# Optimization experiments

Measured on AMD Instinct MI355X. Metric: run time of the kernel, lower is better.

## Reference

```python
import jax, jax.numpy as jnp
import numpy as np

TAU = 0.07
EPS = 1e-10


def setup_inputs() -> dict:
    key = jax.random.key(0)
    k1, k2 = jax.random.split(key)
    N, D = 8192, 128
    features = jax.random.normal(k1, (N, D), dtype=jnp.float32)
    alpha = jnp.float32(0.5)  # cosine-similarity threshold in (-1, 1)
    return {"features": features, "alpha": alpha}


def reference(features, alpha):
    # L2-normalize rows (torch F.normalize uses eps=1e-12 clamp on the norm)
    norm = jnp.maximum(jnp.linalg.norm(features, axis=1, keepdims=True), 1e-12)
    f = features / norm
    sim = f @ f.T  # [N, N]

    n = f.shape[0]
    not_eye = ~jnp.eye(n, dtype=bool)
    pos_mask = (sim >= alpha) & not_eye
    neg_mask = (sim < alpha) & not_eye

    e = jnp.exp(sim / TAU)  # [N, N], computed once and reused for both masks
    numerator = jnp.sum(jnp.where(pos_mask, e, 0.0), axis=1) + EPS
    denominator = numerator + jnp.sum(jnp.where(neg_mask, e, 0.0), axis=1) + EPS
    loss = -jnp.log(numerator / denominator)
    return loss.mean()
```

## Files before the change

### kernel.cpp

```cpp
#include <hip/hip_runtime.h>

#define N_ROWS 8192
#define DIM 128
#define BM 128
#define CHUNK 1024
#define BN 64
#define NITER (CHUNK/BN)
#define NCHUNK (N_ROWS/CHUNK)

typedef __attribute__((ext_vector_type(8))) short short8;
typedef __attribute__((ext_vector_type(4))) float f32x4;

__device__ __forceinline__ void gload_lds16(const void* g, void* l) {
  __builtin_amdgcn_global_load_lds(
      (const __attribute__((address_space(1))) void*)g,
      (__attribute__((address_space(3))) void*)l, 16, 0, 0);
}

__device__ __forceinline__ unsigned short f2bf(float x) {
  unsigned int u = __float_as_uint(x);
  unsigned int r = (u + 0x7fffu + ((u >> 16) & 1u)) >> 16;
  return (unsigned short)r;
}

__global__ __launch_bounds__(256) void knorm(const float* __restrict__ feat,
                                             unsigned int* __restrict__ fn) {
  const int wid = threadIdx.x >> 6;
  const int lane = threadIdx.x & 63;
  const int row = blockIdx.x * 4 + wid;
  const float2 v = *(const float2*)(feat + (size_t)row * DIM + lane * 2);
  float s = v.x * v.x + v.y * v.y;
#pragma unroll
  for (int m = 1; m < 64; m <<= 1) s += __shfl_xor(s, m);
  const float inv = 1.0f / fmaxf(sqrtf(s), 1e-12f);
  const unsigned int pk = (unsigned int)f2bf(v.x * inv) |
                          ((unsigned int)f2bf(v.y * inv) << 16);
  const int chunk = (lane >> 2) ^ (row & 7);
  fn[row * 64 + chunk * 4 + (lane & 3)] = pk;
}

__global__ __launch_bounds__(256, 2) void ksim(const unsigned int* __restrict__ fn,
                                               const float* __restrict__ alphap,
                                               float* __restrict__ posP,
                                               float* __restrict__ totP) {
  __shared__ __align__(16) char smem[65536];
  const int tid = threadIdx.x;
  const int lane = tid & 63;
  const int wid = tid >> 6;
  const int wr = wid >> 1, wc = wid & 1;
  const int r0 = blockIdx.x * BM;
  const int c0 = blockIdx.y * CHUNK;
  const float alpha = alphap[0];
  const float K2 = 14.285714285714286f;

  const char* fbytes = (const char*)fn;

  {
    const char* g = fbytes + (size_t)(r0 + wid * 32 + (lane >> 4)) * 256 + (lane & 15) * 16;
    char* l = smem + wid * 8192;
#pragma unroll
    for (int s = 0; s < 8; s++) gload_lds16(g + s * 1024, l + s * 1024);
  }
  {
    const char* g = fbytes + (size_t)(c0 + wid * 16 + (lane >> 4)) * 256 + (lane & 15) * 16;
    char* l = smem + 32768 + wid * 4096;
#pragma unroll
    for (int s = 0; s < 4; s++) gload_lds16(g + s * 1024, l + s * 1024);
  }
  __syncthreads();

  short8 aR[4][4];
  {
    const int lrb = wr * 64 + (lane & 15);
#pragma unroll
    for (int m = 0; m < 4; m++) {
      const int r = lrb + m * 16;
#pragma unroll
      for (int ks = 0; ks < 4; ks++) {
        const int ch = (ks * 4 + (lane >> 4)) ^ (r & 7);
        aR[m][ks] = *(const short8*)(smem + r * 256 + ch * 16);
      }
    }
  }

  float pp[4][4] = {{0.f}}, tp[4][4] = {{0.f}};
  int cur = 0;

  for (int it = 0; it < NITER; ++it) {
    if (it + 1 < NITER) {
      const int cb = c0 + (it + 1) * BN;
      const char* g = fbytes + (size_t)(cb + wid * 16 + (lane >> 4)) * 256 + (lane & 15) * 16;
      char* l = smem + 32768 + (cur ^ 1) * 16384 + wid * 4096;
#pragma unroll
      for (int s = 0; s < 4; s++) gload_lds16(g + s * 1024, l + s * 1024);
    }

    f32x4 acc[4][2];
#pragma unroll
    for (int m = 0; m < 4; m++)
#pragma unroll
      for (int n = 0; n < 2; n++) acc[m][n] = (f32x4){0.f, 0.f, 0.f, 0.f};

    const char* Bbase = smem + 32768 + cur * 16384;
    const int colA = wc * 32 + (lane & 15);
#pragma unroll
    for (int ks = 0; ks < 4; ks++) {
      const int ch = (ks * 4 + (lane >> 4)) ^ (colA & 7);
      short8 b0 = *(const short8*)(Bbase + colA * 256 + ch * 16);
      short8 b1 = *(const short8*)(Bbase + (colA + 16) * 256 + ch * 16);
#pragma unroll
      for (int m = 0; m < 4; m++) {
        acc[m][0] = __builtin_amdgcn_mfma_f32_16x16x32_bf16(aR[m][ks], b0, acc[m][0], 0, 0, 0);
        acc[m][1] = __builtin_amdgcn_mfma_f32_16x16x32_bf16(aR[m][ks], b1, acc[m][1], 0, 0, 0);
      }
    }

    const int cb = c0 + it * BN;
#pragma unroll
    for (int m = 0; m < 4; m++) {
      const int grb = r0 + wr * 64 + m * 16;
#pragma unroll
      for (int n = 0; n < 2; n++) {
        const int gcb = cb + wc * 32 + n * 16;
        const f32x4 a = acc[m][n];
        if (grb == gcb) {
          const int gr0 = (lane >> 4) << 2;
          const int gcl = lane & 15;
#pragma unroll
          for (int r = 0; r < 4; r++) {
            const float e = __expf(a[r] * K2);
            const float ev = (gr0 + r == gcl) ? 0.0f : e;
            tp[m][r] += ev;
            pp[m][r] += (a[r] >= alpha) ? ev : 0.0f;
          }
        } else {
#pragma unroll
          for (int r = 0; r < 4; r++) {
            const float e = __expf(a[r] * K2);
            tp[m][r] += e;
            pp[m][r] += (a[r] >= alpha) ? e : 0.0f;
          }
        }
      }
    }
    __syncthreads();
    cur ^= 1;
  }

#pragma unroll
  for (int m = 0; m < 4; m++)
#pragma unroll
    for (int r = 0; r < 4; r++) {
      float p = pp[m][r], t = tp[m][r];
#pragma unroll
      for (int msk = 1; msk < 16; msk <<= 1) {
        p += __shfl_xor(p, msk);
        t += __shfl_xor(t, msk);
      }
      pp[m][r] = p;
      tp[m][r] = t;
    }

  float* red = (float*)smem;
  if ((lane & 15) == 0) {
    const int g = lane >> 4;
#pragma unroll
    for (int m = 0; m < 4; m++)
#pragma unroll
      for (int r = 0; r < 4; r++) {
        const int rl = m * 16 + g * 4 + r;
        red[(wid * 64 + rl) * 2 + 0] = pp[m][r];
        red[(wid * 64 + rl) * 2 + 1] = tp[m][r];
      }
  }
  __syncthreads();
  if (tid < BM) {
    const int wrr = tid >> 6, rl = tid & 63;
    const float p = red[((wrr * 2 + 0) * 64 + rl) * 2 + 0] + red[((wrr * 2 + 1) * 64 + rl) * 2 + 0];
    const float t = red[((wrr * 2 + 0) * 64 + rl) * 2 + 1] + red[((wrr * 2 + 1) * 64 + rl) * 2 + 1];
    posP[blockIdx.y * N_ROWS + r0 + tid] = p;
    totP[blockIdx.y * N_ROWS + r0 + tid] = t;
  }
}

__global__ __launch_bounds__(128) void kred1(const float* __restrict__ posP,
                                             const float* __restrict__ totP,
                                             float* __restrict__ bp) {
  const int t = threadIdx.x;
  const int row = blockIdx.x * 128 + t;
  float pos = 0.f, tot = 0.f;
#pragma unroll
  for (int c = 0; c < NCHUNK; c++) {
    pos += posP[c * N_ROWS + row];
    tot += totP[c * N_ROWS + row];
  }
  float term = __logf(tot + 2e-10f) - __logf(pos + 1e-10f);
#pragma unroll
  for (int m = 1; m < 64; m <<= 1) term += __shfl_xor(term, m);
  __shared__ float s2[2];
  if ((t & 63) == 0) s2[t >> 6] = term;
  __syncthreads();
  if (t == 0) bp[blockIdx.x] = s2[0] + s2[1];
}

__global__ void kred2(const float* __restrict__ bp, float* __restrict__ out) {
  const int l = threadIdx.x;
  float v = bp[l];
#pragma unroll
  for (int m = 1; m < 64; m <<= 1) v += __shfl_xor(v, m);
  if (l == 0) out[0] = v * (1.0f / 8192.0f);
}

extern "C" void kernel_launch(void* const* d_in, const int* in_sizes, int n_in,
                              void* d_out, int out_size, void* d_ws, size_t ws_size,
                              hipStream_t stream) {
  const float* feat = (const float*)d_in[0];
  const float* alphap = (const float*)d_in[1];
  char* ws = (char*)d_ws;
  unsigned int* fn = (unsigned int*)ws;
  float* posP = (float*)(ws + (2u << 20));
  float* totP = (float*)(ws + (2u << 20) + (256u << 10));
  float* bp = (float*)(ws + (2u << 20) + (512u << 10));
  float* out = (float*)d_out;

  knorm<<<dim3(N_ROWS / 4), dim3(256), 0, stream>>>(feat, fn);
  ksim<<<dim3(N_ROWS / BM, NCHUNK), dim3(256), 0, stream>>>(fn, alphap, posP, totP);
  kred1<<<dim3(N_ROWS / 128), dim3(128), 0, stream>>>(posP, totP, bp);
  kred2<<<dim3(1), dim3(64), 0, stream>>>(bp, out);
}
```

Measured before the change: 42.50 us.

## Drop LDS staging in similarity kernel, load B directly from global per wave

The similarity kernel no longer stages tiles in shared memory. Each wave loads its own 32 A rows into registers and reads the 64-column B tiles straight from global/L2, which removes all __syncthreads and the cross-wave LDS reduction. CHUNK is halved, which doubles the grid in y, and occupancy is raised to 4 blocks per CU. The exponential now uses the raw v_exp_f32 with a pre-scaled log2e/tau constant. The trade-off is that every wave fetches B redundantly from cache with no latency-hiding prefetch, and doubling the chunks doubles the partial-sum traffic.

```diff
diff --git a/kernel.cpp b/kernel.cpp
--- a/kernel.cpp
+++ b/kernel.cpp
@@ -1,21 +1,14 @@
 #include <hip/hip_runtime.h>
 
 #define N_ROWS 8192
-#define DIM 128
 #define BM 128
-#define CHUNK 1024
+#define CHUNK 512
 #define BN 64
-#define NITER (CHUNK/BN)
-#define NCHUNK (N_ROWS/CHUNK)
+#define NITER (CHUNK / BN)
+#define NCHUNK (N_ROWS / CHUNK)
 
 typedef __attribute__((ext_vector_type(8))) short short8;
 typedef __attribute__((ext_vector_type(4))) float f32x4;
-
-__device__ __forceinline__ void gload_lds16(const void* g, void* l) {
-  __builtin_amdgcn_global_load_lds(
-      (const __attribute__((address_space(1))) void*)g,
-      (__attribute__((address_space(3))) void*)l, 16, 0, 0);
-}
 
 __device__ __forceinline__ unsigned short f2bf(float x) {
   unsigned int u = __float_as_uint(x);
@@ -23,112 +16,92 @@
   return (unsigned short)r;
 }
 
+__device__ __forceinline__ float fast_exp2(float x) {
+  float r;
+  asm("v_exp_f32 %0, %1" : "=v"(r) : "v"(x));
+  return r;
+}
+
 __global__ __launch_bounds__(256) void knorm(const float* __restrict__ feat,
                                              unsigned int* __restrict__ fn) {
   const int wid = threadIdx.x >> 6;
   const int lane = threadIdx.x & 63;
   const int row = blockIdx.x * 4 + wid;
-  const float2 v = *(const float2*)(feat + (size_t)row * DIM + lane * 2);
+  const float2 v = *(const float2*)(feat + (size_t)row * 128 + lane * 2);
   float s = v.x * v.x + v.y * v.y;
 #pragma unroll
   for (int m = 1; m < 64; m <<= 1) s += __shfl_xor(s, m);
   const float inv = 1.0f / fmaxf(sqrtf(s), 1e-12f);
-  const unsigned int pk = (unsigned int)f2bf(v.x * inv) |
-                          ((unsigned int)f2bf(v.y * inv) << 16);
-  const int chunk = (lane >> 2) ^ (row & 7);
-  fn[row * 64 + chunk * 4 + (lane & 3)] = pk;
+  fn[row * 64 + lane] = (unsigned int)f2bf(v.x * inv) |
+                        ((unsigned int)f2bf(v.y * inv) << 16);
 }
 
-__global__ __launch_bounds__(256, 2) void ksim(const unsigned int* __restrict__ fn,
+__global__ __launch_bounds__(256, 4) void ksim(const unsigned int* __restrict__ fn,
                                                const float* __restrict__ alphap,
                                                float* __restrict__ posP,
                                                float* __restrict__ totP) {
-  __shared__ __align__(16) char smem[65536];
   const int tid = threadIdx.x;
   const int lane = tid & 63;
   const int wid = tid >> 6;
-  const int wr = wid >> 1, wc = wid & 1;
   const int r0 = blockIdx.x * BM;
   const int c0 = blockIdx.y * CHUNK;
   const float alpha = alphap[0];
-  const float K2 = 14.285714285714286f;
+  const float KEXP = 20.60992915f;
 
-  const char* fbytes = (const char*)fn;
+  const char* __restrict__ F = (const char*)fn;
 
+  short8 aR[2][4];
   {
-    const char* g = fbytes + (size_t)(r0 + wid * 32 + (lane >> 4)) * 256 + (lane & 15) * 16;
-    char* l = smem + wid * 8192;
+    const char* ar = F + (size_t)(r0 + wid * 32 + (lane & 15)) * 256 + (lane >> 4) * 16;
 #pragma unroll
-    for (int s = 0; s < 8; s++) gload_lds16(g + s * 1024, l + s * 1024);
-  }
-  {
-    const char* g = fbytes + (size_t)(c0 + wid * 16 + (lane >> 4)) * 256 + (lane & 15) * 16;
-    char* l = smem + 32768 + wid * 4096;
+    for (int m = 0; m < 2; m++)
 #pragma unroll
-    for (int s = 0; s < 4; s++) gload_lds16(g + s * 1024, l + s * 1024);
-  }
-  __syncthreads();
-
-  short8 aR[4][4];
-  {
-    const int lrb = wr * 64 + (lane & 15);
-#pragma unroll
-    for (int m = 0; m < 4; m++) {
-      const int r = lrb + m * 16;
-#pragma unroll
-      for (int ks = 0; ks < 4; ks++) {
-        const int ch = (ks * 4 + (lane >> 4)) ^ (r & 7);
-        aR[m][ks] = *(const short8*)(smem + r * 256 + ch * 16);
-      }
-    }
+      for (int ks = 0; ks < 4; ks++)
+        aR[m][ks] = *(const short8*)(ar + m * 16 * 256 + ks * 64);
   }
 
-  float pp[4][4] = {{0.f}}, tp[4][4] = {{0.f}};
-  int cur = 0;
+  float pp[2][4] = {{0.f}}, tp[2][4] = {{0.f}};
+  const char* __restrict__ brow = F + (size_t)(c0 + (lane & 15)) * 256 + (lane >> 4) * 16;
 
+#pragma unroll 1
   for (int it = 0; it < NITER; ++it) {
-    if (it + 1 < NITER) {
-      const int cb = c0 + (it + 1) * BN;
-      const char* g = fbytes + (size_t)(cb + wid * 16 + (lane >> 4)) * 256 + (lane & 15) * 16;
-      char* l = smem + 32768 + (cur ^ 1) * 16384 + wid * 4096;
+    const char* bb = brow + it * (BN * 256);
+
+    f32x4 acc[2][4];
 #pragma unroll
-      for (int s = 0; s < 4; s++) gload_lds16(g + s * 1024, l + s * 1024);
-    }
+    for (int m = 0; m < 2; m++)
+#pragma unroll
+      for (int n = 0; n < 4; n++) acc[m][n] = (f32x4){0.f, 0.f, 0.f, 0.f};
 
-    f32x4 acc[4][2];
-#pragma unroll
-    for (int m = 0; m < 4; m++)
-#pragma unroll
-      for (int n = 0; n < 2; n++) acc[m][n] = (f32x4){0.f, 0.f, 0.f, 0.f};
-
-    const char* Bbase = smem + 32768 + cur * 16384;
-    const int colA = wc * 32 + (lane & 15);
 #pragma unroll
     for (int ks = 0; ks < 4; ks++) {
-      const int ch = (ks * 4 + (lane >> 4)) ^ (colA & 7);
-      short8 b0 = *(const short8*)(Bbase + colA * 256 + ch * 16);
-      short8 b1 = *(const short8*)(Bbase + (colA + 16) * 256 + ch * 16);
+      const short8 b0 = *(const short8*)(bb + 0 * 4096 + ks * 64);
+      const short8 b1 = *(const short8*)(bb + 1 * 4096 + ks * 64);
+      const short8 b2 = *(const short8*)(bb + 2 * 4096 + ks * 64);
+      const short8 b3 = *(const short8*)(bb + 3 * 4096 + ks * 64);
 #pragma unroll
-      for (int m = 0; m < 4; m++) {
+      for (int m = 0; m < 2; m++) {
         acc[m][0] = __builtin_amdgcn_mfma_f32_16x16x32_bf16(aR[m][ks], b0, acc[m][0], 0, 0, 0);
         acc[m][1] = __builtin_amdgcn_mfma_f32_16x16x32_bf16(aR[m][ks], b1, acc[m][1], 0, 0, 0);
+        acc[m][2] = __builtin_amdgcn_mfma_f32_16x16x32_bf16(aR[m][ks], b2, acc[m][2], 0, 0, 0);
+        acc[m][3] = __builtin_amdgcn_mfma_f32_16x16x32_bf16(aR[m][ks], b3, acc[m][3], 0, 0, 0);
       }
     }
 
     const int cb = c0 + it * BN;
 #pragma unroll
-    for (int m = 0; m < 4; m++) {
-      const int grb = r0 + wr * 64 + m * 16;
+    for (int m = 0; m < 2; m++) {
+      const int grb = r0 + wid * 32 + m * 16;
 #pragma unroll
-      for (int n = 0; n < 2; n++) {
-        const int gcb = cb + wc * 32 + n * 16;
+      for (int n = 0; n < 4; n++) {
+        const int gcb = cb + n * 16;
         const f32x4 a = acc[m][n];
         if (grb == gcb) {
           const int gr0 = (lane >> 4) << 2;
           const int gcl = lane & 15;
 #pragma unroll
           for (int r = 0; r < 4; r++) {
-            const float e = __expf(a[r] * K2);
+            const float e = fast_exp2(a[r] * KEXP);
             const float ev = (gr0 + r == gcl) ? 0.0f : e;
             tp[m][r] += ev;
             pp[m][r] += (a[r] >= alpha) ? ev : 0.0f;
@@ -136,19 +109,17 @@
         } else {
 #pragma unroll
           for (int r = 0; r < 4; r++) {
-            const float e = __expf(a[r] * K2);
+            const float e = fast_exp2(a[r] * KEXP);
             tp[m][r] += e;
             pp[m][r] += (a[r] >= alpha) ? e : 0.0f;
           }
         }
       }
     }
-    __syncthreads();
-    cur ^= 1;
   }
 
 #pragma unroll
-  for (int m = 0; m < 4; m++)
+  for (int m = 0; m < 2; m++)
 #pragma unroll
     for (int r = 0; r < 4; r++) {
       float p = pp[m][r], t = tp[m][r];
@@ -157,30 +128,12 @@
         p += __shfl_xor(p, msk);
         t += __shfl_xor(t, msk);
       }
-      pp[m][r] = p;
-      tp[m][r] = t;
+      if ((lane & 15) == 0) {
+        const int row = r0 + wid * 32 + m * 16 + ((lane >> 4) << 2) + r;
+        posP[blockIdx.y * N_ROWS + row] = p;
+        totP[blockIdx.y * N_ROWS + row] = t;
+      }
     }
-
-  float* red = (float*)smem;
-  if ((lane & 15) == 0) {
-    const int g = lane >> 4;
-#pragma unroll
-    for (int m = 0; m < 4; m++)
-#pragma unroll
-      for (int r = 0; r < 4; r++) {
-        const int rl = m * 16 + g * 4 + r;
-        red[(wid * 64 + rl) * 2 + 0] = pp[m][r];
-        red[(wid * 64 + rl) * 2 + 1] = tp[m][r];
-      }
-  }
-  __syncthreads();
-  if (tid < BM) {
-    const int wrr = tid >> 6, rl = tid & 63;
-    const float p = red[((wrr * 2 + 0) * 64 + rl) * 2 + 0] + red[((wrr * 2 + 1) * 64 + rl) * 2 + 0];
-    const float t = red[((wrr * 2 + 0) * 64 + rl) * 2 + 1] + red[((wrr * 2 + 1) * 64 + rl) * 2 + 1];
-    posP[blockIdx.y * N_ROWS + r0 + tid] = p;
-    totP[blockIdx.y * N_ROWS + r0 + tid] = t;
-  }
 }
 
 __global__ __launch_bounds__(128) void kred1(const float* __restrict__ posP,
@@ -219,8 +172,8 @@
   char* ws = (char*)d_ws;
   unsigned int* fn = (unsigned int*)ws;
   float* posP = (float*)(ws + (2u << 20));
-  float* totP = (float*)(ws + (2u << 20) + (256u << 10));
-  float* bp = (float*)(ws + (2u << 20) + (512u << 10));
+  float* totP = (float*)(ws + (2u << 20) + (512u << 10));
+  float* bp = (float*)(ws + (3u << 20));
   float* out = (float*)d_out;
 
   knorm<<<dim3(N_ROWS / 4), dim3(256), 0, stream>>>(feat, fn);
```

After: 77.37 us. 1.82x slower.

## Fold exp scale into prescaled A operand, halve chunk, drop block reduction

Applied to the files above, without the earlier changes.

The A rows are pre-multiplied by 1/(tau*ln2) in bf16, so the MFMA output can go straight into a raw v_exp_f32 (exp2) with no per-element multiply. The threshold alpha is scaled by the same factor. A fragments now load directly from global memory into registers instead of through LDS, which halves shared memory and lets occupancy rise to 3 blocks per CU. CHUNK is halved for more blocks, and the cross-wave LDS reduction is replaced by per-wave partial writes that kred1 sums. The bf16 rounding of the prescaled values can shift results near the alpha threshold slightly, and knorm now writes two copies of the normalized features.

```diff
diff --git a/kernel.cpp b/kernel.cpp
--- a/kernel.cpp
+++ b/kernel.cpp
@@ -1,12 +1,13 @@
 #include <hip/hip_runtime.h>
 
 #define N_ROWS 8192
-#define DIM 128
 #define BM 128
-#define CHUNK 1024
+#define CHUNK 512
 #define BN 64
-#define NITER (CHUNK/BN)
-#define NCHUNK (N_ROWS/CHUNK)
+#define NITER (CHUNK / BN)
+#define NCHUNK (N_ROWS / CHUNK)
+#define NPART (NCHUNK * 2)
+#define KEXP 20.60992915f
 
 typedef __attribute__((ext_vector_type(8))) short short8;
 typedef __attribute__((ext_vector_type(4))) float f32x4;
@@ -23,74 +24,73 @@
   return (unsigned short)r;
 }
 
+__device__ __forceinline__ float fast_exp2(float x) {
+  float r;
+  asm("v_exp_f32 %0, %1" : "=v"(r) : "v"(x));
+  return r;
+}
+
 __global__ __launch_bounds__(256) void knorm(const float* __restrict__ feat,
-                                             unsigned int* __restrict__ fn) {
+                                             unsigned int* __restrict__ fnA,
+                                             unsigned int* __restrict__ fnB) {
   const int wid = threadIdx.x >> 6;
   const int lane = threadIdx.x & 63;
   const int row = blockIdx.x * 4 + wid;
-  const float2 v = *(const float2*)(feat + (size_t)row * DIM + lane * 2);
+  const float2 v = *(const float2*)(feat + (size_t)row * 128 + lane * 2);
   float s = v.x * v.x + v.y * v.y;
 #pragma unroll
   for (int m = 1; m < 64; m <<= 1) s += __shfl_xor(s, m);
   const float inv = 1.0f / fmaxf(sqrtf(s), 1e-12f);
-  const unsigned int pk = (unsigned int)f2bf(v.x * inv) |
-                          ((unsigned int)f2bf(v.y * inv) << 16);
-  const int chunk = (lane >> 2) ^ (row & 7);
-  fn[row * 64 + chunk * 4 + (lane & 3)] = pk;
-}
-
-__global__ __launch_bounds__(256, 2) void ksim(const unsigned int* __restrict__ fn,
+  const float x = v.x * inv, y = v.y * inv;
+  const int idx = row * 64 + ((lane >> 2) ^ (row & 7)) * 4 + (lane & 3);
+  fnB[idx] = (unsigned int)f2bf(x) | ((unsigned int)f2bf(y) << 16);
+  fnA[idx] = (unsigned int)f2bf(x * KEXP) | ((unsigned int)f2bf(y * KEXP) << 16);
+}
+
+__global__ __launch_bounds__(256, 3) void ksim(const unsigned int* __restrict__ fnA,
+                                               const unsigned int* __restrict__ fnB,
                                                const float* __restrict__ alphap,
                                                float* __restrict__ posP,
                                                float* __restrict__ totP) {
-  __shared__ __align__(16) char smem[65536];
+  __shared__ __align__(16) char smem[32768];
   const int tid = threadIdx.x;
   const int lane = tid & 63;
   const int wid = tid >> 6;
   const int wr = wid >> 1, wc = wid & 1;
   const int r0 = blockIdx.x * BM;
   const int c0 = blockIdx.y * CHUNK;
-  const float alpha = alphap[0];
-  const float K2 = 14.285714285714286f;
-
-  const char* fbytes = (const char*)fn;
+  const float alphaK = alphap[0] * KEXP;
+
+  const char* __restrict__ FA = (const char*)fnA;
+  const char* __restrict__ FB = (const char*)fnB;
+
+  short8 aR[4][4];
+#pragma unroll
+  for (int m = 0; m < 4; m++) {
+    const int r = r0 + wr * 64 + m * 16 + (lane & 15);
+#pragma unroll
+    for (int ks = 0; ks < 4; ks++) {
+      const int ch = (ks * 4 + (lane >> 4)) ^ (r & 7);
+      aR[m][ks] = *(const short8*)(FA + (size_t)r * 256 + ch * 16);
+    }
+  }
 
   {
-    const char* g = fbytes + (size_t)(r0 + wid * 32 + (lane >> 4)) * 256 + (lane & 15) * 16;
-    char* l = smem + wid * 8192;
-#pragma unroll
-    for (int s = 0; s < 8; s++) gload_lds16(g + s * 1024, l + s * 1024);
-  }
-  {
-    const char* g = fbytes + (size_t)(c0 + wid * 16 + (lane >> 4)) * 256 + (lane & 15) * 16;
-    char* l = smem + 32768 + wid * 4096;
+    const char* g = FB + (size_t)(c0 + wid * 16 + (lane >> 4)) * 256 + (lane & 15) * 16;
+    char* l = smem + wid * 4096;
 #pragma unroll
     for (int s = 0; s < 4; s++) gload_lds16(g + s * 1024, l + s * 1024);
   }
   __syncthreads();
-
-  short8 aR[4][4];
-  {
-    const int lrb = wr * 64 + (lane & 15);
-#pragma unroll
-    for (int m = 0; m < 4; m++) {
-      const int r = lrb + m * 16;
-#pragma unroll
-      for (int ks = 0; ks < 4; ks++) {
-        const int ch = (ks * 4 + (lane >> 4)) ^ (r & 7);
-        aR[m][ks] = *(const short8*)(smem + r * 256 + ch * 16);
-      }
-    }
-  }
 
   float pp[4][4] = {{0.f}}, tp[4][4] = {{0.f}};
   int cur = 0;
 
+#pragma unroll 1
   for (int it = 0; it < NITER; ++it) {
     if (it + 1 < NITER) {
-      const int cb = c0 + (it + 1) * BN;
-      const char* g = fbytes + (size_t)(cb + wid * 16 + (lane >> 4)) * 256 + (lane & 15) * 16;
-      char* l = smem + 32768 + (cur ^ 1) * 16384 + wid * 4096;
+      const char* g = FB + (size_t)(c0 + (it + 1) * BN + wid * 16 + (lane >> 4)) * 256 + (lane & 15) * 16;
+      char* l = smem + (cur ^ 1) * 16384 + wid * 4096;
 #pragma unroll
       for (int s = 0; s < 4; s++) gload_lds16(g + s * 1024, l + s * 1024);
     }
@@ -101,13 +101,13 @@
 #pragma unroll
       for (int n = 0; n < 2; n++) acc[m][n] = (f32x4){0.f, 0.f, 0.f, 0.f};
 
-    const char* Bbase = smem + 32768 + cur * 16384;
-    const int colA = wc * 32 + (lane & 15);
+    const char* Bb = smem + cur * 16384;
 #pragma unroll
     for (int ks = 0; ks < 4; ks++) {
-      const int ch = (ks * 4 + (lane >> 4)) ^ (colA & 7);
-      short8 b0 = *(const short8*)(Bbase + colA * 256 + ch * 16);
-      short8 b1 = *(const short8*)(Bbase + (colA + 16) * 256 + ch * 16);
+      const int rB0 = wc * 32 + (lane & 15);
+      const int ch = (ks * 4 + (lane >> 4)) ^ (lane & 7);
+      const short8 b0 = *(const short8*)(Bb + rB0 * 256 + ch * 16);
+      const short8 b1 = *(const short8*)(Bb + (rB0 + 16) * 256 + ch * 16);
 #pragma unroll
       for (int m = 0; m < 4; m++) {
         acc[m][0] = __builtin_amdgcn_mfma_f32_16x16x32_bf16(aR[m][ks], b0, acc[m][0], 0, 0, 0);
@@ -128,17 +128,17 @@
           const int gcl = lane & 15;
 #pragma unroll
           for (int r = 0; r < 4; r++) {
-            const float e = __expf(a[r] * K2);
+            const float e = fast_exp2(a[r]);
             const float ev = (gr0 + r == gcl) ? 0.0f : e;
             tp[m][r] += ev;
-            pp[m][r] += (a[r] >= alpha) ? ev : 0.0f;
+            pp[m][r] += (a[r] >= alphaK) ? ev : 0.0f;
           }
         } else {
 #pragma unroll
           for (int r = 0; r < 4; r++) {
-            const float e = __expf(a[r] * K2);
+            const float e = fast_exp2(a[r]);
             tp[m][r] += e;
-            pp[m][r] += (a[r] >= alpha) ? e : 0.0f;
+            pp[m][r] += (a[r] >= alphaK) ? e : 0.0f;
           }
         }
       }
@@ -157,30 +157,13 @@
         p += __shfl_xor(p, msk);
         t += __shfl_xor(t, msk);
       }
-      pp[m][r] = p;
-      tp[m][r] = t;
-    }
-
-  float* red = (float*)smem;
-  if ((lane & 15) == 0) {
-    const int g = lane >> 4;
-#pragma unroll
-    for (int m = 0; m < 4; m++)
-#pragma unroll
-      for (int r = 0; r < 4; r++) {
-        const int rl = m * 16 + g * 4 + r;
-        red[(wid * 64 + rl) * 2 + 0] = pp[m][r];
-        red[(wid * 64 + rl) * 2 + 1] = tp[m][r];
-      }
-  }
-  __syncthreads();
-  if (tid < BM) {
-    const int wrr = tid >> 6, rl = tid & 63;
-    const float p = red[((wrr * 2 + 0) * 64 + rl) * 2 + 0] + red[((wrr * 2 + 1) * 64 + rl) * 2 + 0];
-    const float t = red[((wrr * 2 + 0) * 64 + rl) * 2 + 1] + red[((wrr * 2 + 1) * 64 + rl) * 2 + 1];
-    posP[blockIdx.y * N_ROWS + r0 + tid] = p;
-    totP[blockIdx.y * N_ROWS + r0 + tid] = t;
-  }
+      if ((lane & 15) == 0) {
+        const int row = r0 + wr * 64 + m * 16 + ((lane >> 4) << 2) + r;
+        const int part = blockIdx.y * 2 + wc;
+        posP[part * N_ROWS + row] = p;
+        totP[part * N_ROWS + row] = t;
+      }
+    }
 }
 
 __global__ __launch_bounds__(128) void kred1(const float* __restrict__ posP,
@@ -190,7 +173,7 @@
   const int row = blockIdx.x * 128 + t;
   float pos = 0.f, tot = 0.f;
 #pragma unroll
-  for (int c = 0; c < NCHUNK; c++) {
+  for (int c = 0; c < NPART; c++) {
     pos += posP[c * N_ROWS + row];
     tot += totP[c * N_ROWS + row];
   }
@@ -217,14 +200,15 @@
   const float* feat = (const float*)d_in[0];
   const float* alphap = (const float*)d_in[1];
   char* ws = (char*)d_ws;
-  unsigned int* fn = (unsigned int*)ws;
-  float* posP = (float*)(ws + (2u << 20));
-  float* totP = (float*)(ws + (2u << 20) + (256u << 10));
-  float* bp = (float*)(ws + (2u << 20) + (512u << 10));
+  unsigned int* fnA = (unsigned int*)ws;
+  unsigned int* fnB = (unsigned int*)(ws + (2u << 20));
+  float* posP = (float*)(ws + (4u << 20));
+  float* totP = (float*)(ws + (5u << 20));
+  float* bp = (float*)(ws + (6u << 20));
   float* out = (float*)d_out;
 
-  knorm<<<dim3(N_ROWS / 4), dim3(256), 0, stream>>>(feat, fn);
-  ksim<<<dim3(N_ROWS / BM, NCHUNK), dim3(256), 0, stream>>>(fn, alphap, posP, totP);
+  knorm<<<dim3(N_ROWS / 4), dim3(256), 0, stream>>>(feat, fnA, fnB);
+  ksim<<<dim3(N_ROWS / BM, NCHUNK), dim3(256), 0, stream>>>(fnA, fnB, alphap, posP, totP);
   kred1<<<dim3(N_ROWS / 128), dim3(128), 0, stream>>>(posP, totP, bp);
   kred2<<<dim3(1), dim3(64), 0, stream>>>(bp, out);
 }
```

Result: slower. 69.91 us (+64.5%).
